# Performance work log

Measured on AMD Instinct MI355X. Metric: run time of the kernel, lower is better.

Reference implementation:

```python
import jax, jax.numpy as jnp
import numpy as np

EMBED = 1024
N_HEADS = 16
HEAD_DIM = EMBED // N_HEADS
B, T = 2, 2048


def setup_inputs() -> dict:
    key = jax.random.key(0)
    k1, k2, k3 = jax.random.split(key, 3)
    x = jax.random.normal(k1, (B, T, EMBED), dtype=jnp.float32)
    # torch nn.Linear(embed, 3*embed, bias=False): weight [3C, C]; store as [C, 3C] for x @ W
    w_attn = jax.random.normal(k2, (EMBED, 3 * EMBED), dtype=jnp.float32) * (EMBED ** -0.5)
    w_proj = jax.random.normal(k3, (EMBED, EMBED), dtype=jnp.float32) * (EMBED ** -0.5)
    return {"x": x, "w_attn": w_attn, "w_proj": w_proj}


def reference(x, w_attn, w_proj):
    Bb, Tt, C = x.shape
    kqv = x @ w_attn  # [B, T, 3C]
    # NOTE: original code unpacks as k, q, v (k first)
    k, q, v = jnp.split(kqv, 3, axis=2)
    def heads(t):
        return t.reshape(Bb, Tt, N_HEADS, HEAD_DIM).transpose(0, 2, 1, 3)  # [B, H, T, D]
    k, q, v = heads(k), heads(q), heads(v)
    scale = HEAD_DIM ** -0.5
    wei = jnp.einsum("bhqd,bhkd->bhqk", q, k) * scale  # [B, H, T, T]
    mask = jnp.tril(jnp.ones((Tt, Tt), dtype=bool))
    wei = jnp.where(mask[None, None], wei, -jnp.inf)
    wei = jax.nn.softmax(wei, axis=-1)
    y = jnp.einsum("bhqk,bhkd->bhqd", wei, v)  # [B, H, T, D]
    y = y.transpose(0, 2, 1, 3).reshape(Bb, Tt, C)
    return y @ w_proj
```

## Files before the change

kernel.cpp:

```cpp
#include <hip/hip_runtime.h>

typedef unsigned short u16;
typedef unsigned int u32;

typedef __attribute__((ext_vector_type(4))) float f32x4;
typedef __attribute__((ext_vector_type(8))) short s16x8;
typedef __attribute__((ext_vector_type(4))) u32 u32x4;

__device__ __forceinline__ u16 f2bf(float f) {
    u32 u = __builtin_bit_cast(u32, f);
    u += 0x7fffu + ((u >> 16) & 1u);
    return (u16)(u >> 16);
}

__device__ __forceinline__ u32 pk_bf16(float a, float b) {
    return (u32)f2bf(a) | ((u32)f2bf(b) << 16);
}

__device__ __forceinline__ u32 cvtpk(float a, float b) {
    u32 r;
    asm("v_cvt_pk_bf16_f32 %0, %1, %2" : "=v"(r) : "v"(a), "v"(b));
    return r;
}

__device__ __forceinline__ float bf2f(u16 h) {
    u32 u = ((u32)h) << 16;
    return __builtin_bit_cast(float, u);
}

__device__ __forceinline__ void pl32swap(u32& a, u32& b) {
    asm volatile("v_permlane32_swap_b32 %0, %1" : "+v"(a), "+v"(b));
}
__device__ __forceinline__ void pl16swap(u32& a, u32& b) {
    asm volatile("v_permlane16_swap_b32 %0, %1" : "+v"(a), "+v"(b));
}

#define EXP2(x) exp2f(x)

__device__ __forceinline__ void gload16(const u16* g, u16* l) {
    __builtin_amdgcn_global_load_lds(
        (const __attribute__((address_space(1))) void*)(const void*)g,
        (__attribute__((address_space(3))) void*)(void*)l, 16, 0, 0);
}

__global__ void k_cast(const float* __restrict__ in, u16* __restrict__ out) {
    int i = (blockIdx.x * 256 + threadIdx.x) * 4;
    float4 v = *(const float4*)(in + i);
    uint2 pk;
    pk.x = pk_bf16(v.x, v.y);
    pk.y = pk_bf16(v.z, v.w);
    *(uint2*)(out + i) = pk;
}

__global__ void k_transpose(const float* __restrict__ in, u16* __restrict__ out,
                            int K, int N) {
    __shared__ float tile[32][33];
    int n0 = blockIdx.x * 32, k0 = blockIdx.y * 32;
    int x = threadIdx.x, y = threadIdx.y;
#pragma unroll
    for (int j = 0; j < 32; j += 8)
        tile[y + j][x] = in[(size_t)(k0 + y + j) * N + n0 + x];
    __syncthreads();
#pragma unroll
    for (int j = 0; j < 32; j += 8)
        out[(size_t)(n0 + y + j) * K + k0 + x] = f2bf(tile[x][y + j]);
}

template <int EPI>
__global__ __launch_bounds__(256, 2) void k_gemm(
        const u16* __restrict__ A, const u16* __restrict__ Bt,
        void* __restrict__ Cout, u16* __restrict__ Vt, int N, int K) {
    __shared__ u16 As[128 * 32];
    __shared__ u16 Bs[128 * 32];
    const int nbn = N >> 7;
    const int cpx = (int)gridDim.x >> 3;
    const int bid = (int)blockIdx.x;
    const int swb = (bid & 7) * cpx + (bid >> 3);
    const int bm = swb / nbn, bn = swb % nbn;
    const int tid = threadIdx.x;
    const int wv = tid >> 6, ln = tid & 63;
    const int lg = ln >> 4, lr = ln & 15;
    const int wr = (wv >> 1) << 6, wc = (wv & 1) << 6;

    const u16* gA = A + (size_t)(bm * 128 + wv * 32 + (ln >> 2)) * K + (ln & 3) * 8;
    const u16* gB = Bt + (size_t)(bn * 128 + wv * 32 + (ln >> 2)) * K + (ln & 3) * 8;
    u16* lA = As + wv * 1024;
    u16* lB = Bs + wv * 1024;

    f32x4 acc[4][4] = {};

    for (int k0 = 0; k0 < K; k0 += 32) {
        gload16(gA + k0, lA);
        gload16(gA + k0 + 16 * K, lA + 512);
        gload16(gB + k0, lB);
        gload16(gB + k0 + 16 * K, lB + 512);
        __syncthreads();
        s16x8 af[4], bf[4];
#pragma unroll
        for (int mi = 0; mi < 4; ++mi)
            af[mi] = *(const s16x8*)&As[(wr + mi * 16 + lr) * 32 + lg * 8];
#pragma unroll
        for (int ni = 0; ni < 4; ++ni)
            bf[ni] = *(const s16x8*)&Bs[(wc + ni * 16 + lr) * 32 + lg * 8];
#pragma unroll
        for (int mi = 0; mi < 4; ++mi)
#pragma unroll
            for (int ni = 0; ni < 4; ++ni)
                acc[mi][ni] = __builtin_amdgcn_mfma_f32_16x16x32_bf16(
                        af[mi], bf[ni], acc[mi][ni], 0, 0, 0);
        __syncthreads();
    }

    const int crow0 = bm * 128 + wr + lg * 4;
    const int ccol0 = bn * 128 + wc + lr;
    if (EPI == 0) {
        float* Co = (float*)Cout;
#pragma unroll
        for (int mi = 0; mi < 4; ++mi)
#pragma unroll
            for (int ni = 0; ni < 4; ++ni)
#pragma unroll
                for (int r = 0; r < 4; ++r)
                    Co[(size_t)(crow0 + mi * 16 + r) * N + ccol0 + ni * 16] =
                            acc[mi][ni][r];
    } else {
        if (bn < 16) {
            const float qs = (bn >= 8) ? 0.18033688011112042f : 1.0f;
            u16* Co = (u16*)Cout;
#pragma unroll
            for (int mi = 0; mi < 4; ++mi)
#pragma unroll
                for (int ni = 0; ni < 4; ++ni)
#pragma unroll
                    for (int r = 0; r < 4; ++r)
                        Co[(size_t)(crow0 + mi * 16 + r) * 3072 + ccol0 + ni * 16] =
                                f2bf(acc[mi][ni][r] * qs);
        } else {
#pragma unroll
            for (int mi = 0; mi < 4; ++mi) {
                int row = crow0 + mi * 16;
                int bb = row >> 11, t = row & 2047;
#pragma unroll
                for (int ni = 0; ni < 4; ++ni) {
                    int hd = ccol0 + ni * 16 - 2048;
                    uint2 pk;
                    pk.x = pk_bf16(acc[mi][ni][0], acc[mi][ni][1]);
                    pk.y = pk_bf16(acc[mi][ni][2], acc[mi][ni][3]);
                    *(uint2*)&Vt[(size_t)(bb * 1024 + hd) * 2048 + t] = pk;
                }
            }
        }
    }
}

__global__ __launch_bounds__(512, 4) void k_attn(
        const u16* __restrict__ kqv, const u16* __restrict__ Vt,
        u16* __restrict__ y) {
    const int orig = blockIdx.x;
    const int xcd = orig & 7, slot = orig >> 3;
    const int bh = xcd * 4 + (slot >> 4);
    const int pr = slot & 15;
    const int b = bh >> 4, h = bh & 15;
    const int tid = threadIdx.x;
    const int wave = tid >> 6;
    const int g = wave >> 2;
    const int wv4 = wave & 3;
    const int lane = tid & 63;
    const int lg = lane >> 4, lr = lane & 15;

    __shared__ u16 Ks[2][2][64 * 64];
    __shared__ u16 Vs[2][2][64 * 64];
    __shared__ u16 comb[4 * 64 * 20];

    const u16* Kg = kqv + (size_t)b * 2048 * 3072 + h * 64;
    const u16* Qg = Kg + 1024;
    const u16* Vg = Vt + (size_t)bh * 64 * 2048;

    const int srow = wv4 * 16 + (lane >> 3);
    const int cK = (lane & 7) ^ (lane >> 3);
    const u16* kg0 = Kg + (size_t)srow * 3072 + cK * 8;
    const u16* vg0 = Vg + (size_t)srow * 2048 + cK * 8;
    const int swz = lr & 7;

    s16x8 ones;
#pragma unroll
    for (int i = 0; i < 8; ++i) ones[i] = (short)0x3F80;

#define STAGE(bb, t)                                      \
    {                                                     \
        const u16* kp_ = kg0 + (size_t)(t) * 64 * 3072;   \
        const u16* vp_ = vg0 + (size_t)(t) * 64;          \
        u16* lk_ = &Ks[g][bb][wv4 * 1024];                \
        u16* lv_ = &Vs[g][bb][wv4 * 1024];                \
        gload16(kp_, lk_);                                \
        gload16(kp_ + 8 * 3072, lk_ + 512);               \
        gload16(vp_, lv_);                                \
        gload16(vp_ + 8 * 2048, lv_ + 512);               \
    }

    for (int pass = 0; pass < 2; ++pass) {
        const int qt = pass ? (31 - pr) : pr;
        const int nkt = qt + 1;
        const int iters = (nkt + 1) >> 1;
        const int qbase = qt * 64 + wv4 * 16;

        const u16* qrp = Qg + (size_t)(qbase + lr) * 3072;
        const s16x8 qf0 = *(const s16x8*)(qrp + lg * 8);
        const s16x8 qf1 = *(const s16x8*)(qrp + 32 + lg * 8);

        f32x4 o[4] = {};
        f32x4 l4 = {};

        if (g < nkt) STAGE(0, g);
        asm volatile("s_waitcnt vmcnt(0)\n\ts_barrier" ::: "memory");

        for (int i = 0; i < iters; ++i) {
            const int cur = i & 1;
            const int t = 2 * i + g;
            if (t + 2 < nkt) STAGE(cur ^ 1, t + 2);
            if (t < nkt) {
                f32x4 st[4];
                __builtin_amdgcn_s_setprio(1);
#pragma unroll
                for (int kb = 0; kb < 4; ++kb) {
                    const int row = kb * 16 + lr;
                    s16x8 kf0 = *(const s16x8*)&Ks[g][cur][row * 64 + ((lg ^ swz) << 3)];
                    s16x8 kf1 = *(const s16x8*)&Ks[g][cur][row * 64 + (((4 + lg) ^ swz) << 3)];
                    f32x4 z = {};
                    z = __builtin_amdgcn_mfma_f32_16x16x32_bf16(kf0, qf0, z, 0, 0, 0);
                    z = __builtin_amdgcn_mfma_f32_16x16x32_bf16(kf1, qf1, z, 0, 0, 0);
                    st[kb] = z;
                }
                __builtin_amdgcn_s_setprio(0);

                if (t == nkt - 1) {
                    const int q_abs = qbase + lr;
                    const int kb0 = t * 64 + lg * 4;
#pragma unroll
                    for (int kb = 0; kb < 4; ++kb)
#pragma unroll
                        for (int r = 0; r < 4; ++r)
                            st[kb][r] = EXP2((kb0 + kb * 16 + r <= q_abs)
                                                 ? st[kb][r] : -3e38f);
                } else {
#pragma unroll
                    for (int kb = 0; kb < 4; ++kb)
#pragma unroll
                        for (int r = 0; r < 4; ++r) st[kb][r] = EXP2(st[kb][r]);
                }

                u32 E[2][2], O[2][2];
#pragma unroll
                for (int kbh = 0; kbh < 2; ++kbh)
#pragma unroll
                    for (int hh = 0; hh < 2; ++hh) {
                        E[kbh][hh] = cvtpk(st[2 * kbh][2 * hh], st[2 * kbh][2 * hh + 1]);
                        O[kbh][hh] = cvtpk(st[2 * kbh + 1][2 * hh], st[2 * kbh + 1][2 * hh + 1]);
                    }
#pragma unroll
                for (int kbh = 0; kbh < 2; ++kbh)
#pragma unroll
                    for (int hh = 0; hh < 2; ++hh) {
                        pl32swap(E[kbh][hh], O[kbh][hh]);
                        pl16swap(E[kbh][hh], O[kbh][hh]);
                    }

                __builtin_amdgcn_s_setprio(1);
#pragma unroll
                for (int half = 0; half < 2; ++half) {
                    u32x4 pw;
                    pw.x = E[half][0];
                    pw.y = E[half][1];
                    pw.z = O[half][0];
                    pw.w = O[half][1];
                    s16x8 pf = __builtin_bit_cast(s16x8, pw);
                    l4 = __builtin_amdgcn_mfma_f32_16x16x32_bf16(ones, pf, l4, 0, 0, 0);
#pragma unroll
                    for (int dt = 0; dt < 4; ++dt) {
                        const int vrow = dt * 16 + lr;
                        s16x8 vf = *(const s16x8*)&Vs[g][cur][vrow * 64 +
                                                    (((half * 4 + lg) ^ swz) << 3)];
                        o[dt] = __builtin_amdgcn_mfma_f32_16x16x32_bf16(vf, pf, o[dt], 0, 0, 0);
                    }
                }
                __builtin_amdgcn_s_setprio(0);
            }
            asm volatile("s_waitcnt vmcnt(0)\n\ts_barrier" ::: "memory");
        }

        if (g == 1) {
            u16* ce = comb + (size_t)(wv4 * 64 + lane) * 20;
#pragma unroll
            for (int dt = 0; dt < 4; ++dt) {
                uint2 w;
                w.x = cvtpk(o[dt][0], o[dt][1]);
                w.y = cvtpk(o[dt][2], o[dt][3]);
                *(uint2*)(ce + dt * 4) = w;
            }
            *(float*)(ce + 16) = l4[0];
        }
        __syncthreads();
        if (g == 0) {
            const u16* ce = comb + (size_t)(wv4 * 64 + lane) * 20;
            float l = l4[0] + *(const float*)(ce + 16);
#pragma unroll
            for (int dt = 0; dt < 4; ++dt) {
                uint2 w = *(const uint2*)(ce + dt * 4);
                o[dt][0] += bf2f((u16)(w.x & 0xffff));
                o[dt][1] += bf2f((u16)(w.x >> 16));
                o[dt][2] += bf2f((u16)(w.y & 0xffff));
                o[dt][3] += bf2f((u16)(w.y >> 16));
            }
            const float inv = 1.0f / l;
            u16* yb = y + (size_t)(b * 2048 + qbase + lr) * 1024 + h * 64;
#pragma unroll
            for (int dt = 0; dt < 4; ++dt) {
                uint2 w;
                w.x = cvtpk(o[dt][0] * inv, o[dt][1] * inv);
                w.y = cvtpk(o[dt][2] * inv, o[dt][3] * inv);
                *(uint2*)(yb + dt * 16 + lg * 4) = w;
            }
        }
        __syncthreads();
    }
#undef STAGE
}

extern "C" void kernel_launch(void* const* d_in, const int* in_sizes, int n_in,
                              void* d_out, int out_size, void* d_ws, size_t ws_size,
                              hipStream_t stream) {
    const float* x = (const float*)d_in[0];
    const float* w_attn = (const float*)d_in[1];
    const float* w_proj = (const float*)d_in[2];
    float* out = (float*)d_out;
    char* ws = (char*)d_ws;

    u16* x_bf = (u16*)(ws);
    u16* wat  = (u16*)(ws + (size_t)(8 << 20));
    u16* wpt  = (u16*)(ws + (size_t)(14 << 20));
    u16* kqv  = (u16*)(ws + (size_t)(16 << 20));
    u16* vt   = (u16*)(ws + (size_t)(40 << 20));
    u16* yb   = (u16*)(ws + (size_t)(48 << 20));

    k_cast<<<4096, 256, 0, stream>>>(x, x_bf);
    k_transpose<<<dim3(96, 32), dim3(32, 8), 0, stream>>>(w_attn, wat, 1024, 3072);
    k_transpose<<<dim3(32, 32), dim3(32, 8), 0, stream>>>(w_proj, wpt, 1024, 1024);
    k_gemm<1><<<32 * 24, 256, 0, stream>>>(x_bf, wat, kqv, vt, 3072, 1024);
    k_attn<<<512, 512, 0, stream>>>(kqv, vt, yb);
    k_gemm<0><<<32 * 8, 256, 0, stream>>>(yb, wpt, out, nullptr, 1024, 1024);
}
```

Baseline: 172.0 us.

## Merge prep kernels, split attention into one q-tile per block, shrink proj GEMM tile

Folds the cast and two weight transposes into a single prep launch. The attention kernel drops the two-group split-K with LDS combine and paired q-tiles: each 256-thread block now handles a single q-tile with a simple double-buffered K/V loop, launched as 1024 blocks with a rotated tile order for causal balance. The output projection GEMM uses 64x128 tiles with 512 blocks to fill more CUs. Giving up the intra-block split over K tiles lengthens the serial per-block loop for late q-tiles, in exchange for no combine step and more blocks.

```diff
diff --git a/kernel.cpp b/kernel.cpp
--- a/kernel.cpp
+++ b/kernel.cpp
@@ -23,11 +23,6 @@
     return r;
 }
 
-__device__ __forceinline__ float bf2f(u16 h) {
-    u32 u = ((u32)h) << 16;
-    return __builtin_bit_cast(float, u);
-}
-
 __device__ __forceinline__ void pl32swap(u32& a, u32& b) {
     asm volatile("v_permlane32_swap_b32 %0, %1" : "+v"(a), "+v"(b));
 }
@@ -43,33 +38,46 @@
         (__attribute__((address_space(3))) void*)(void*)l, 16, 0, 0);
 }
 
-__global__ void k_cast(const float* __restrict__ in, u16* __restrict__ out) {
-    int i = (blockIdx.x * 256 + threadIdx.x) * 4;
-    float4 v = *(const float4*)(in + i);
-    uint2 pk;
-    pk.x = pk_bf16(v.x, v.y);
-    pk.y = pk_bf16(v.z, v.w);
-    *(uint2*)(out + i) = pk;
-}
-
-__global__ void k_transpose(const float* __restrict__ in, u16* __restrict__ out,
-                            int K, int N) {
+__global__ void k_prep(const float* __restrict__ x, u16* __restrict__ x_bf,
+                       const float* __restrict__ wa, u16* __restrict__ wat,
+                       const float* __restrict__ wp, u16* __restrict__ wpt) {
+    const int bid = blockIdx.x;
+    const int tid = threadIdx.x;
+    if (bid < 4096) {
+        int i = (bid * 256 + tid) * 4;
+        float4 v = *(const float4*)(x + i);
+        uint2 pk;
+        pk.x = pk_bf16(v.x, v.y);
+        pk.y = pk_bf16(v.z, v.w);
+        *(uint2*)(x_bf + i) = pk;
+        return;
+    }
+    const float* in;
+    u16* out;
+    int n0, k0, N;
+    if (bid < 4096 + 3072) {
+        int loc = bid - 4096;
+        in = wa; out = wat; N = 3072;
+        n0 = (loc % 96) * 32; k0 = (loc / 96) * 32;
+    } else {
+        int loc = bid - 4096 - 3072;
+        in = wp; out = wpt; N = 1024;
+        n0 = (loc & 31) * 32; k0 = (loc >> 5) * 32;
+    }
     __shared__ float tile[32][33];
-    int n0 = blockIdx.x * 32, k0 = blockIdx.y * 32;
-    int x = threadIdx.x, y = threadIdx.y;
+    const int tx = tid & 31, ty = tid >> 5;
 #pragma unroll
     for (int j = 0; j < 32; j += 8)
-        tile[y + j][x] = in[(size_t)(k0 + y + j) * N + n0 + x];
+        tile[ty + j][tx] = in[(size_t)(k0 + ty + j) * N + n0 + tx];
     __syncthreads();
 #pragma unroll
     for (int j = 0; j < 32; j += 8)
-        out[(size_t)(n0 + y + j) * K + k0 + x] = f2bf(tile[x][y + j]);
-}
-
-template <int EPI>
-__global__ __launch_bounds__(256, 2) void k_gemm(
+        out[(size_t)(n0 + ty + j) * 1024 + k0 + tx] = f2bf(tile[tx][ty + j]);
+}
+
+__global__ __launch_bounds__(256, 2) void k_gemm1(
         const u16* __restrict__ A, const u16* __restrict__ Bt,
-        void* __restrict__ Cout, u16* __restrict__ Vt, int N, int K) {
+        u16* __restrict__ Cout, u16* __restrict__ Vt, int N, int K) {
     __shared__ u16 As[128 * 32];
     __shared__ u16 Bs[128 * 32];
     const int nbn = N >> 7;
@@ -113,217 +121,222 @@
 
     const int crow0 = bm * 128 + wr + lg * 4;
     const int ccol0 = bn * 128 + wc + lr;
-    if (EPI == 0) {
-        float* Co = (float*)Cout;
+    if (bn < 16) {
+        const float qs = (bn >= 8) ? 0.18033688011112042f : 1.0f;
 #pragma unroll
         for (int mi = 0; mi < 4; ++mi)
 #pragma unroll
             for (int ni = 0; ni < 4; ++ni)
 #pragma unroll
                 for (int r = 0; r < 4; ++r)
-                    Co[(size_t)(crow0 + mi * 16 + r) * N + ccol0 + ni * 16] =
-                            acc[mi][ni][r];
+                    Cout[(size_t)(crow0 + mi * 16 + r) * 3072 + ccol0 + ni * 16] =
+                            f2bf(acc[mi][ni][r] * qs);
     } else {
-        if (bn < 16) {
-            const float qs = (bn >= 8) ? 0.18033688011112042f : 1.0f;
-            u16* Co = (u16*)Cout;
-#pragma unroll
-            for (int mi = 0; mi < 4; ++mi)
-#pragma unroll
-                for (int ni = 0; ni < 4; ++ni)
-#pragma unroll
-                    for (int r = 0; r < 4; ++r)
-                        Co[(size_t)(crow0 + mi * 16 + r) * 3072 + ccol0 + ni * 16] =
-                                f2bf(acc[mi][ni][r] * qs);
-        } else {
-#pragma unroll
-            for (int mi = 0; mi < 4; ++mi) {
-                int row = crow0 + mi * 16;
-                int bb = row >> 11, t = row & 2047;
-#pragma unroll
-                for (int ni = 0; ni < 4; ++ni) {
-                    int hd = ccol0 + ni * 16 - 2048;
-                    uint2 pk;
-                    pk.x = pk_bf16(acc[mi][ni][0], acc[mi][ni][1]);
-                    pk.y = pk_bf16(acc[mi][ni][2], acc[mi][ni][3]);
-                    *(uint2*)&Vt[(size_t)(bb * 1024 + hd) * 2048 + t] = pk;
-                }
+#pragma unroll
+        for (int mi = 0; mi < 4; ++mi) {
+            int row = crow0 + mi * 16;
+            int bb = row >> 11, t = row & 2047;
+#pragma unroll
+            for (int ni = 0; ni < 4; ++ni) {
+                int hd = ccol0 + ni * 16 - 2048;
+                uint2 pk;
+                pk.x = pk_bf16(acc[mi][ni][0], acc[mi][ni][1]);
+                pk.y = pk_bf16(acc[mi][ni][2], acc[mi][ni][3]);
+                *(uint2*)&Vt[(size_t)(bb * 1024 + hd) * 2048 + t] = pk;
             }
         }
     }
 }
 
-__global__ __launch_bounds__(512, 4) void k_attn(
+__global__ __launch_bounds__(256, 4) void k_gemm2(
+        const u16* __restrict__ A, const u16* __restrict__ Bt,
+        float* __restrict__ Co, int N, int K) {
+    __shared__ u16 As[64 * 32];
+    __shared__ u16 Bs[128 * 32];
+    const int nbn = N >> 7;
+    const int cpx = (int)gridDim.x >> 3;
+    const int bid = (int)blockIdx.x;
+    const int swb = (bid & 7) * cpx + (bid >> 3);
+    const int bm = swb / nbn, bn = swb % nbn;
+    const int tid = threadIdx.x;
+    const int wv = tid >> 6, ln = tid & 63;
+    const int lg = ln >> 4, lr = ln & 15;
+
+    const u16* gA = A + (size_t)(bm * 64 + wv * 16 + (ln >> 2)) * K + (ln & 3) * 8;
+    const u16* gB = Bt + (size_t)(bn * 128 + wv * 32 + (ln >> 2)) * K + (ln & 3) * 8;
+    u16* lA = As + wv * 512;
+    u16* lB = Bs + wv * 1024;
+
+    f32x4 acc[4][2] = {};
+
+    for (int k0 = 0; k0 < K; k0 += 32) {
+        gload16(gA + k0, lA);
+        gload16(gB + k0, lB);
+        gload16(gB + k0 + 16 * K, lB + 512);
+        __syncthreads();
+        s16x8 af[4], bf[2];
+#pragma unroll
+        for (int mi = 0; mi < 4; ++mi)
+            af[mi] = *(const s16x8*)&As[(mi * 16 + lr) * 32 + lg * 8];
+#pragma unroll
+        for (int ni = 0; ni < 2; ++ni)
+            bf[ni] = *(const s16x8*)&Bs[(wv * 32 + ni * 16 + lr) * 32 + lg * 8];
+#pragma unroll
+        for (int mi = 0; mi < 4; ++mi)
+#pragma unroll
+            for (int ni = 0; ni < 2; ++ni)
+                acc[mi][ni] = __builtin_amdgcn_mfma_f32_16x16x32_bf16(
+                        af[mi], bf[ni], acc[mi][ni], 0, 0, 0);
+        __syncthreads();
+    }
+
+    const int crow0 = bm * 64 + lg * 4;
+    const int ccol0 = bn * 128 + wv * 32 + lr;
+#pragma unroll
+    for (int mi = 0; mi < 4; ++mi)
+#pragma unroll
+        for (int ni = 0; ni < 2; ++ni)
+#pragma unroll
+            for (int r = 0; r < 4; ++r)
+                Co[(size_t)(crow0 + mi * 16 + r) * N + ccol0 + ni * 16] =
+                        acc[mi][ni][r];
+}
+
+__global__ __launch_bounds__(256, 4) void k_attn(
         const u16* __restrict__ kqv, const u16* __restrict__ Vt,
         u16* __restrict__ y) {
     const int orig = blockIdx.x;
     const int xcd = orig & 7, slot = orig >> 3;
-    const int bh = xcd * 4 + (slot >> 4);
-    const int pr = slot & 15;
+    const int bh_l = slot >> 5, q_i = slot & 31;
+    const int bh = xcd * 4 + bh_l;
+    const int qt = 31 - ((q_i + 8 * bh_l) & 31);
     const int b = bh >> 4, h = bh & 15;
     const int tid = threadIdx.x;
-    const int wave = tid >> 6;
-    const int g = wave >> 2;
-    const int wv4 = wave & 3;
-    const int lane = tid & 63;
+    const int wave = tid >> 6, lane = tid & 63;
     const int lg = lane >> 4, lr = lane & 15;
 
-    __shared__ u16 Ks[2][2][64 * 64];
-    __shared__ u16 Vs[2][2][64 * 64];
-    __shared__ u16 comb[4 * 64 * 20];
+    __shared__ u16 Ks[2][64 * 64];
+    __shared__ u16 Vs[2][64 * 64];
 
     const u16* Kg = kqv + (size_t)b * 2048 * 3072 + h * 64;
     const u16* Qg = Kg + 1024;
     const u16* Vg = Vt + (size_t)bh * 64 * 2048;
 
-    const int srow = wv4 * 16 + (lane >> 3);
     const int cK = (lane & 7) ^ (lane >> 3);
-    const u16* kg0 = Kg + (size_t)srow * 3072 + cK * 8;
-    const u16* vg0 = Vg + (size_t)srow * 2048 + cK * 8;
+    const u16* kg0 = Kg + (size_t)(wave * 16 + (lane >> 3)) * 3072 + cK * 8;
+    const u16* vg0 = Vg + (size_t)(wave * 16 + (lane >> 3)) * 2048 + cK * 8;
     const int swz = lr & 7;
 
+    const int nkt = qt + 1;
+    const int qbase = qt * 64 + wave * 16;
+
+    const u16* qrp = Qg + (size_t)(qbase + lr) * 3072;
+    const s16x8 qf0 = *(const s16x8*)(qrp + lg * 8);
+    const s16x8 qf1 = *(const s16x8*)(qrp + 32 + lg * 8);
+
     s16x8 ones;
 #pragma unroll
     for (int i = 0; i < 8; ++i) ones[i] = (short)0x3F80;
 
-#define STAGE(bb, t)                                      \
-    {                                                     \
-        const u16* kp_ = kg0 + (size_t)(t) * 64 * 3072;   \
-        const u16* vp_ = vg0 + (size_t)(t) * 64;          \
-        u16* lk_ = &Ks[g][bb][wv4 * 1024];                \
-        u16* lv_ = &Vs[g][bb][wv4 * 1024];                \
-        gload16(kp_, lk_);                                \
-        gload16(kp_ + 8 * 3072, lk_ + 512);               \
-        gload16(vp_, lv_);                                \
-        gload16(vp_ + 8 * 2048, lv_ + 512);               \
-    }
-
-    for (int pass = 0; pass < 2; ++pass) {
-        const int qt = pass ? (31 - pr) : pr;
-        const int nkt = qt + 1;
-        const int iters = (nkt + 1) >> 1;
-        const int qbase = qt * 64 + wv4 * 16;
-
-        const u16* qrp = Qg + (size_t)(qbase + lr) * 3072;
-        const s16x8 qf0 = *(const s16x8*)(qrp + lg * 8);
-        const s16x8 qf1 = *(const s16x8*)(qrp + 32 + lg * 8);
-
-        f32x4 o[4] = {};
-        f32x4 l4 = {};
-
-        if (g < nkt) STAGE(0, g);
-        asm volatile("s_waitcnt vmcnt(0)\n\ts_barrier" ::: "memory");
-
-        for (int i = 0; i < iters; ++i) {
-            const int cur = i & 1;
-            const int t = 2 * i + g;
-            if (t + 2 < nkt) STAGE(cur ^ 1, t + 2);
-            if (t < nkt) {
-                f32x4 st[4];
-                __builtin_amdgcn_s_setprio(1);
-#pragma unroll
-                for (int kb = 0; kb < 4; ++kb) {
-                    const int row = kb * 16 + lr;
-                    s16x8 kf0 = *(const s16x8*)&Ks[g][cur][row * 64 + ((lg ^ swz) << 3)];
-                    s16x8 kf1 = *(const s16x8*)&Ks[g][cur][row * 64 + (((4 + lg) ^ swz) << 3)];
-                    f32x4 z = {};
-                    z = __builtin_amdgcn_mfma_f32_16x16x32_bf16(kf0, qf0, z, 0, 0, 0);
-                    z = __builtin_amdgcn_mfma_f32_16x16x32_bf16(kf1, qf1, z, 0, 0, 0);
-                    st[kb] = z;
-                }
-                __builtin_amdgcn_s_setprio(0);
-
-                if (t == nkt - 1) {
-                    const int q_abs = qbase + lr;
-                    const int kb0 = t * 64 + lg * 4;
-#pragma unroll
-                    for (int kb = 0; kb < 4; ++kb)
-#pragma unroll
-                        for (int r = 0; r < 4; ++r)
-                            st[kb][r] = EXP2((kb0 + kb * 16 + r <= q_abs)
-                                                 ? st[kb][r] : -3e38f);
-                } else {
-#pragma unroll
-                    for (int kb = 0; kb < 4; ++kb)
-#pragma unroll
-                        for (int r = 0; r < 4; ++r) st[kb][r] = EXP2(st[kb][r]);
-                }
-
-                u32 E[2][2], O[2][2];
-#pragma unroll
-                for (int kbh = 0; kbh < 2; ++kbh)
-#pragma unroll
-                    for (int hh = 0; hh < 2; ++hh) {
-                        E[kbh][hh] = cvtpk(st[2 * kbh][2 * hh], st[2 * kbh][2 * hh + 1]);
-                        O[kbh][hh] = cvtpk(st[2 * kbh + 1][2 * hh], st[2 * kbh + 1][2 * hh + 1]);
-                    }
-#pragma unroll
-                for (int kbh = 0; kbh < 2; ++kbh)
-#pragma unroll
-                    for (int hh = 0; hh < 2; ++hh) {
-                        pl32swap(E[kbh][hh], O[kbh][hh]);
-                        pl16swap(E[kbh][hh], O[kbh][hh]);
-                    }
-
-                __builtin_amdgcn_s_setprio(1);
-#pragma unroll
-                for (int half = 0; half < 2; ++half) {
-                    u32x4 pw;
-                    pw.x = E[half][0];
-                    pw.y = E[half][1];
-                    pw.z = O[half][0];
-                    pw.w = O[half][1];
-                    s16x8 pf = __builtin_bit_cast(s16x8, pw);
-                    l4 = __builtin_amdgcn_mfma_f32_16x16x32_bf16(ones, pf, l4, 0, 0, 0);
-#pragma unroll
-                    for (int dt = 0; dt < 4; ++dt) {
-                        const int vrow = dt * 16 + lr;
-                        s16x8 vf = *(const s16x8*)&Vs[g][cur][vrow * 64 +
-                                                    (((half * 4 + lg) ^ swz) << 3)];
-                        o[dt] = __builtin_amdgcn_mfma_f32_16x16x32_bf16(vf, pf, o[dt], 0, 0, 0);
-                    }
-                }
-                __builtin_amdgcn_s_setprio(0);
+    f32x4 o[4] = {};
+    f32x4 l4 = {};
+
+#define STAGE(bb, t)                                          \
+    {                                                         \
+        const u16* kp_ = kg0 + (size_t)(t) * 64 * 3072;       \
+        const u16* vp_ = vg0 + (size_t)(t) * 64;              \
+        gload16(kp_, &Ks[bb][wave * 1024]);                   \
+        gload16(kp_ + 8 * 3072, &Ks[bb][wave * 1024 + 512]);  \
+        gload16(vp_, &Vs[bb][wave * 1024]);                   \
+        gload16(vp_ + 8 * 2048, &Vs[bb][wave * 1024 + 512]);  \
+    }
+
+    STAGE(0, 0);
+    asm volatile("s_waitcnt vmcnt(0)\n\ts_barrier" ::: "memory");
+
+    for (int t = 0; t < nkt; ++t) {
+        const int cur = t & 1;
+        if (t + 1 < nkt) STAGE(cur ^ 1, t + 1);
+
+        f32x4 st[4];
+        __builtin_amdgcn_s_setprio(1);
+#pragma unroll
+        for (int kb = 0; kb < 4; ++kb) {
+            const int row = kb * 16 + lr;
+            s16x8 kf0 = *(const s16x8*)&Ks[cur][row * 64 + ((lg ^ swz) << 3)];
+            s16x8 kf1 = *(const s16x8*)&Ks[cur][row * 64 + (((4 + lg) ^ swz) << 3)];
+            f32x4 z = {};
+            z = __builtin_amdgcn_mfma_f32_16x16x32_bf16(kf0, qf0, z, 0, 0, 0);
+            z = __builtin_amdgcn_mfma_f32_16x16x32_bf16(kf1, qf1, z, 0, 0, 0);
+            st[kb] = z;
+        }
+        __builtin_amdgcn_s_setprio(0);
+
+        if (t == nkt - 1) {
+            const int q_abs = qbase + lr;
+            const int kb0 = t * 64 + lg * 4;
+#pragma unroll
+            for (int kb = 0; kb < 4; ++kb)
+#pragma unroll
+                for (int r = 0; r < 4; ++r)
+                    st[kb][r] = EXP2((kb0 + kb * 16 + r <= q_abs)
+                                         ? st[kb][r] : -3e38f);
+        } else {
+#pragma unroll
+            for (int kb = 0; kb < 4; ++kb)
+#pragma unroll
+                for (int r = 0; r < 4; ++r) st[kb][r] = EXP2(st[kb][r]);
+        }
+
+        u32 E[2][2], O[2][2];
+#pragma unroll
+        for (int kbh = 0; kbh < 2; ++kbh)
+#pragma unroll
+            for (int hh = 0; hh < 2; ++hh) {
+                E[kbh][hh] = cvtpk(st[2 * kbh][2 * hh], st[2 * kbh][2 * hh + 1]);
+                O[kbh][hh] = cvtpk(st[2 * kbh + 1][2 * hh], st[2 * kbh + 1][2 * hh + 1]);
             }
-            asm volatile("s_waitcnt vmcnt(0)\n\ts_barrier" ::: "memory");
-        }
-
-        if (g == 1) {
-            u16* ce = comb + (size_t)(wv4 * 64 + lane) * 20;
+#pragma unroll
+        for (int kbh = 0; kbh < 2; ++kbh)
+#pragma unroll
+            for (int hh = 0; hh < 2; ++hh) {
+                pl32swap(E[kbh][hh], O[kbh][hh]);
+                pl16swap(E[kbh][hh], O[kbh][hh]);
+            }
+
+        __builtin_amdgcn_s_setprio(1);
+#pragma unroll
+        for (int half = 0; half < 2; ++half) {
+            u32x4 pw;
+            pw.x = E[half][0];
+            pw.y = E[half][1];
+            pw.z = O[half][0];
+            pw.w = O[half][1];
+            s16x8 pf = __builtin_bit_cast(s16x8, pw);
+            l4 = __builtin_amdgcn_mfma_f32_16x16x32_bf16(ones, pf, l4, 0, 0, 0);
 #pragma unroll
             for (int dt = 0; dt < 4; ++dt) {
-                uint2 w;
-                w.x = cvtpk(o[dt][0], o[dt][1]);
-                w.y = cvtpk(o[dt][2], o[dt][3]);
-                *(uint2*)(ce + dt * 4) = w;
-            }
-            *(float*)(ce + 16) = l4[0];
-        }
-        __syncthreads();
-        if (g == 0) {
-            const u16* ce = comb + (size_t)(wv4 * 64 + lane) * 20;
-            float l = l4[0] + *(const float*)(ce + 16);
-#pragma unroll
-            for (int dt = 0; dt < 4; ++dt) {
-                uint2 w = *(const uint2*)(ce + dt * 4);
-                o[dt][0] += bf2f((u16)(w.x & 0xffff));
-                o[dt][1] += bf2f((u16)(w.x >> 16));
-                o[dt][2] += bf2f((u16)(w.y & 0xffff));
-                o[dt][3] += bf2f((u16)(w.y >> 16));
-            }
-            const float inv = 1.0f / l;
-            u16* yb = y + (size_t)(b * 2048 + qbase + lr) * 1024 + h * 64;
-#pragma unroll
-            for (int dt = 0; dt < 4; ++dt) {
-                uint2 w;
-                w.x = cvtpk(o[dt][0] * inv, o[dt][1] * inv);
-                w.y = cvtpk(o[dt][2] * inv, o[dt][3] * inv);
-                *(uint2*)(yb + dt * 16 + lg * 4) = w;
+                const int vrow = dt * 16 + lr;
+                s16x8 vf = *(const s16x8*)&Vs[cur][vrow * 64 +
+                                                   (((half * 4 + lg) ^ swz) << 3)];
+                o[dt] = __builtin_amdgcn_mfma_f32_16x16x32_bf16(vf, pf, o[dt], 0, 0, 0);
             }
         }
-        __syncthreads();
+        __builtin_amdgcn_s_setprio(0);
+
+        asm volatile("s_waitcnt vmcnt(0)\n\ts_barrier" ::: "memory");
     }
 #undef STAGE
+
+    const float inv = 1.0f / l4[0];
+    u16* yb = y + (size_t)(b * 2048 + qbase + lr) * 1024 + h * 64;
+#pragma unroll
+    for (int dt = 0; dt < 4; ++dt) {
+        uint2 w;
+        w.x = cvtpk(o[dt][0] * inv, o[dt][1] * inv);
+        w.y = cvtpk(o[dt][2] * inv, o[dt][3] * inv);
+        *(uint2*)(yb + dt * 16 + lg * 4) = w;
+    }
 }
 
 extern "C" void kernel_launch(void* const* d_in, const int* in_sizes, int n_in,
@@ -342,10 +355,9 @@
     u16* vt   = (u16*)(ws + (size_t)(40 << 20));
     u16* yb   = (u16*)(ws + (size_t)(48 << 20));
 
-    k_cast<<<4096, 256, 0, stream>>>(x, x_bf);
-    k_transpose<<<dim3(96, 32), dim3(32, 8), 0, stream>>>(w_attn, wat, 1024, 3072);
-    k_transpose<<<dim3(32, 32), dim3(32, 8), 0, stream>>>(w_proj, wpt, 1024, 1024);
-    k_gemm<1><<<32 * 24, 256, 0, stream>>>(x_bf, wat, kqv, vt, 3072, 1024);
-    k_attn<<<512, 512, 0, stream>>>(kqv, vt, yb);
-    k_gemm<0><<<32 * 8, 256, 0, stream>>>(yb, wpt, out, nullptr, 1024, 1024);
-}
+    k_prep<<<4096 + 3072 + 1024, 256, 0, stream>>>(x, x_bf, w_attn, wat,
+                                                   w_proj, wpt);
+    k_gemm1<<<32 * 24, 256, 0, stream>>>(x_bf, wat, kqv, vt, 3072, 1024);
+    k_attn<<<1024, 256, 0, stream>>>(kqv, vt, yb);
+    k_gemm2<<<64 * 8, 256, 0, stream>>>(yb, wpt, out, 1024, 1024);
+}
```

Result: slower. 176.9 us (+2.8%).
